# Optimization experiments

Hardware: AMD Instinct MI355X
Metric: run time of the kernel (lower is better)

The kernel has to match this reference:

```python
import jax, jax.numpy as jnp
import numpy as np

ALPHA = 0.2          # LeakyReLU negative slope (Alpha)
NEG_INF = -9e15      # mask value used by pygat-style GAT


def _masked_attention(Wh, a_src, a_dst, mask):
    """Wh: [H,N,d], a_src/a_dst: [H,d], mask: [N,N] (nonzero = edge).
    Returns attention-aggregated features [H,N,d]."""
    f_src = jnp.einsum('hnd,hd->hn', Wh, a_src)   # [H,N]
    f_dst = jnp.einsum('hnd,hd->hn', Wh, a_dst)   # [H,N]
    e = jax.nn.leaky_relu(f_src[:, :, None] + f_dst[:, None, :], ALPHA)  # [H,N,N]
    e = jnp.where(mask[None, :, :] > 0, e, NEG_INF)
    att = jax.nn.softmax(e, axis=-1)              # masked softmax over neighbors
    return jnp.einsum('hnm,hmd->hnd', att, Wh)    # [H,N,d]


def setup_inputs() -> dict:
    key = jax.random.key(0)
    ks = jax.random.split(key, 8)
    N, F_in, D, H = 4096, 512, 64, 8
    x = jax.random.normal(ks[0], (N, F_in), dtype=jnp.float32)
    adj = jax.random.randint(ks[1], (N, N), 0, 2, dtype=jnp.int32)
    s = 0.1
    W = jax.random.normal(ks[2], (H, F_in, D), dtype=jnp.float32) * s
    a_src = jax.random.normal(ks[3], (H, D), dtype=jnp.float32) * s
    a_dst = jax.random.normal(ks[4], (H, D), dtype=jnp.float32) * s
    W_o = jax.random.normal(ks[5], (H * D, D), dtype=jnp.float32) * s
    ao_src = jax.random.normal(ks[6], (D,), dtype=jnp.float32) * s
    ao_dst = jax.random.normal(ks[7], (D,), dtype=jnp.float32) * s
    return {"x": x, "adj": adj, "W": W, "a_src": a_src, "a_dst": a_dst,
            "W_o": W_o, "ao_src": ao_src, "ao_dst": ao_dst}


def reference(x, adj, W, a_src, a_dst, W_o, ao_src, ao_dst):
    N = x.shape[0]
    # --- multi-head layer (concat=True: ELU per head, concat on feature dim) ---
    Wh = jnp.einsum('nf,hfd->hnd', x, W)                     # [H,N,d]
    h1 = jax.nn.elu(_masked_attention(Wh, a_src, a_dst, adj))  # [H,N,d]
    h_cat = jnp.transpose(h1, (1, 0, 2)).reshape(N, -1)      # [N, H*d]
    # --- output head (concat=False: no ELU inside layer) ---
    Who = (h_cat @ W_o)[None]                                # [1,N,d]
    h2 = _masked_attention(Who, ao_src[None], ao_dst[None], adj)[0]  # [N,d]
    # GAT.forward: activation (ELU) then log_softmax over dim=1
    return jax.nn.log_softmax(jax.nn.elu(h2), axis=1)
```

## Files before the change

### kernel.cpp

```cpp
#include <hip/hip_runtime.h>
#include <hip/hip_bf16.h>
#include <math.h>

#define N_NODES 4096
#define FDIM 512
#define D 64
#define H 8
#define NWORDS (N_NODES / 64)
#define S1 4
#define S2 16

typedef __attribute__((ext_vector_type(8))) short bf16x8;
typedef __attribute__((ext_vector_type(4))) float f32x4;
typedef __attribute__((ext_vector_type(8))) _Float16 f16x8;
typedef __attribute__((ext_vector_type(2))) _Float16 f16x2;
typedef __attribute__((ext_vector_type(4))) unsigned int u32x4;

__device__ inline short f2h(float x) {
    _Float16 h = (_Float16)x;
    return __builtin_bit_cast(short, h);
}
__device__ inline float h2f(unsigned short u) {
    return (float)__builtin_bit_cast(_Float16, u);
}
__device__ inline f16x2 bcH(unsigned int u) { return __builtin_bit_cast(f16x2, u); }

__device__ inline int sext_bit(unsigned int v, int j) {
#if defined(__has_builtin) && __has_builtin(__builtin_amdgcn_sbfe)
    return __builtin_amdgcn_sbfe((int)v, j, 1);
#else
    return ((int)(v << (31 - j))) >> 31;
#endif
}

__device__ inline unsigned fenc(float f) {
    unsigned u = __builtin_bit_cast(unsigned, f);
    return (u & 0x80000000u) ? ~u : (u | 0x80000000u);
}
__device__ inline float fdec(unsigned e) {
    unsigned u = (e & 0x80000000u) ? (e & 0x7FFFFFFFu) : ~e;
    return __builtin_bit_cast(float, u);
}

__device__ inline void gl2lds16(const void* g, void* l) {
#if defined(__has_builtin) && __has_builtin(__builtin_amdgcn_global_load_lds)
    __builtin_amdgcn_global_load_lds(
        (const __attribute__((address_space(1))) unsigned int*)g,
        (__attribute__((address_space(3))) unsigned int*)l, 16, 0, 0);
#else
    *(uint4*)l = *(const uint4*)g;
#endif
}

#define NB_BITS (N_NODES * N_NODES / 2048)
#define NB_X    (N_NODES * FDIM / 1024)
#define NB_W    (H * FDIM * D / 256)
#define NB_WO   (FDIM * D / 256)
__global__ void k_pre(const int* __restrict__ adj, const float* __restrict__ x,
                      const float* __restrict__ W, const float* __restrict__ Wo,
                      unsigned int* __restrict__ bits32, short* __restrict__ Xbf,
                      short* __restrict__ WF, short* __restrict__ WoF,
                      float* __restrict__ cm1, float* __restrict__ cm2,
                      unsigned* __restrict__ gmaxe1, unsigned* __restrict__ gmaxe2) {
    const int b = blockIdx.x, t = threadIdx.x;
    if (b == 0) {
        for (int i = t; i < H * D; i += 256) cm1[i] = 0.f;
        if (t < D) cm2[t] = 0.f;
        if (t < H) gmaxe1[t] = 0u;
        if (t == 0) gmaxe2[0] = 0u;
        return;
    }
    if (b < 1 + NB_BITS) {
        const int tid  = (b - 1) * 256 + t;
        const size_t e0 = (size_t)tid * 8;
        int4 a0 = *(const int4*)&adj[e0];
        int4 a1 = *(const int4*)&adj[e0 + 4];
        unsigned by = (unsigned)(a0.x != 0)       | ((unsigned)(a0.y != 0) << 1)
                    | ((unsigned)(a0.z != 0) << 2) | ((unsigned)(a0.w != 0) << 3)
                    | ((unsigned)(a1.x != 0) << 4) | ((unsigned)(a1.y != 0) << 5)
                    | ((unsigned)(a1.z != 0) << 6) | ((unsigned)(a1.w != 0) << 7);
        unsigned v = by | (__shfl_xor((int)by, 1) << 8);
        v = v | ((unsigned)__shfl_xor((int)v, 2) << 16);
        if ((t & 3) == 0) bits32[tid >> 2] = v;
        return;
    }
    if (b < 1 + NB_BITS + NB_X) {
        const size_t i4 = ((size_t)(b - 1 - NB_BITS) * 256 + t) * 4;
        float4 v = *(const float4*)&x[i4];
        ushort4 o;
        o.x = (unsigned short)f2h(v.x); o.y = (unsigned short)f2h(v.y);
        o.z = (unsigned short)f2h(v.z); o.w = (unsigned short)f2h(v.w);
        *(ushort4*)&Xbf[i4] = o;
        return;
    }
    if (b < 1 + NB_BITS + NB_X + NB_W) {
        const size_t idx = (size_t)(b - 1 - NB_BITS - NB_X) * 256 + t;
        const int d = idx & 63;
        const int k = (int)(idx >> 6) & 511;
        const int h = (int)(idx >> 15);
        WF[(((size_t)h * 64 + (k >> 3)) * 64 + d) * 8 + (k & 7)] = f2h(W[idx]);
        return;
    }
    {
        const size_t idx = (size_t)(b - 1 - NB_BITS - NB_X - NB_W) * 256 + t;
        const int d = idx & 63;
        const int k = (int)(idx >> 6);
        WoF[(((size_t)(k >> 3)) * 64 + d) * 8 + (k & 7)] = f2h(Wo[idx]);
    }
}

__global__ void __launch_bounds__(256) k_gemm(
    const short* __restrict__ Xbf, const short* __restrict__ WF,
    const float* __restrict__ av, const float* __restrict__ bv,
    short* __restrict__ WBout, float* __restrict__ fs, float* __restrict__ fd,
    unsigned* __restrict__ gmaxe, float* __restrict__ cm) {
    const int h  = blockIdx.y;
    const int i0 = blockIdx.x * 64;
    const int t = threadIdx.x, w = t >> 6, lane = t & 63;
    const int li = lane & 15, quad = lane >> 4, k0 = quad * 8;
    const int row_a = i0 + w * 16 + li;
    const short* __restrict__ Xr  = Xbf + (size_t)row_a * FDIM;
    const short* __restrict__ WFh = WF + (size_t)h * 64 * D * 8;

    f32x4 c0 = {0.f, 0.f, 0.f, 0.f}, c1 = c0, c2 = c0, c3 = c0;
    #pragma unroll 4
    for (int kt = 0; kt < FDIM; kt += 32) {
        f16x8 a = __builtin_bit_cast(f16x8, *(const bf16x8*)&Xr[kt + k0]);
        const short* bb = WFh + (size_t)((kt >> 3) + quad) * (D * 8) + li * 8;
        f16x8 b0 = __builtin_bit_cast(f16x8, *(const bf16x8*)(bb));
        f16x8 b1 = __builtin_bit_cast(f16x8, *(const bf16x8*)(bb + 128));
        f16x8 b2 = __builtin_bit_cast(f16x8, *(const bf16x8*)(bb + 256));
        f16x8 b3 = __builtin_bit_cast(f16x8, *(const bf16x8*)(bb + 384));
        c0 = __builtin_amdgcn_mfma_f32_16x16x32_f16(a, b0, c0, 0, 0, 0);
        c1 = __builtin_amdgcn_mfma_f32_16x16x32_f16(a, b1, c1, 0, 0, 0);
        c2 = __builtin_amdgcn_mfma_f32_16x16x32_f16(a, b2, c2, 0, 0, 0);
        c3 = __builtin_amdgcn_mfma_f32_16x16x32_f16(a, b3, c3, 0, 0, 0);
    }
    float av4[4], bv4[4];
    #pragma unroll
    for (int t4 = 0; t4 < 4; ++t4) {
        av4[t4] = av[h * D + t4 * 16 + li];
        bv4[t4] = bv[h * D + t4 * 16 + li];
    }
    float tiles[4][4];
    #pragma unroll
    for (int r = 0; r < 4; ++r) { tiles[0][r] = c0[r]; tiles[1][r] = c1[r]; tiles[2][r] = c2[r]; tiles[3][r] = c3[r]; }

    __shared__ float csum[4][64];
    __shared__ float red[4];
    float fdmax = -INFINITY;
    float s4[4] = {0.f, 0.f, 0.f, 0.f};

    #pragma unroll
    for (int r = 0; r < 4; ++r) {
        const int row = i0 + w * 16 + quad * 4 + r;
        float pa = 0.f, pb = 0.f;
        #pragma unroll
        for (int t4 = 0; t4 < 4; ++t4) {
            const float v = tiles[t4][r];
            const int d = t4 * 16 + li;
            WBout[((size_t)h * (N_NODES / 8) + (row >> 3)) * (D * 8) + d * 8 + (row & 7)] = f2h(v);
            pa += v * av4[t4];
            pb += v * bv4[t4];
            s4[t4] += v;
        }
        #pragma unroll
        for (int off = 1; off < 16; off <<= 1) {
            pa += __shfl_xor(pa, off);
            pb += __shfl_xor(pb, off);
        }
        if (li == 0) {
            fs[(size_t)h * N_NODES + row] = pa;
            fd[(size_t)h * N_NODES + row] = pb;
        }
        fdmax = fmaxf(fdmax, pb);
    }
    fdmax = fmaxf(fdmax, __shfl_xor(fdmax, 16));
    fdmax = fmaxf(fdmax, __shfl_xor(fdmax, 32));
    if (lane == 0) red[w] = fdmax;
    #pragma unroll
    for (int t4 = 0; t4 < 4; ++t4) {
        s4[t4] += __shfl_xor(s4[t4], 16);
        s4[t4] += __shfl_xor(s4[t4], 32);
    }
    if (quad == 0)
        #pragma unroll
        for (int t4 = 0; t4 < 4; ++t4) csum[w][t4 * 16 + li] = s4[t4];
    __syncthreads();
    if (t == 0)
        atomicMax(gmaxe + h, fenc(fmaxf(fmaxf(red[0], red[1]), fmaxf(red[2], red[3]))));
    if (t < 64)
        atomicAdd(&cm[h * D + t],
                  (csum[0][t] + csum[1][t] + csum[2][t] + csum[3][t]) * (1.f / (float)N_NODES));
}

__global__ void __launch_bounds__(128, 2) k_accum(
    const unsigned int* __restrict__ bits32,
    const short* __restrict__ WB,
    const float* __restrict__ fsb, const float* __restrict__ fdb,
    const unsigned* __restrict__ gmaxe,
    short* __restrict__ num, float* __restrict__ den, int kslab) {

    __shared__ __align__(16) short Bt[2][16 * 64 * 8];
    __shared__ __align__(16) short Esh[1024];
    __shared__ __align__(16) short Gsh[1024];

    const int h = blockIdx.y, i0 = blockIdx.x * 128, slab = blockIdx.z;
    const int t = threadIdx.x, w = t >> 6, lane = t & 63;
    const int li = lane & 15, quad = lane >> 4, k0 = quad * 8;
    const size_t ho = (size_t)h * N_NODES;
    const float  gm = fdec(gmaxe[h]);
    const float* __restrict__ fd = fdb + ho;
    const short* __restrict__ Bh = WB + (size_t)h * (N_NODES / 8) * D * 8;

    const int k_beg = slab * kslab;
    const int ntile = kslab / 128;

    auto stage = [&](int buf, int jtile) {
        const short* src = Bh + (size_t)(jtile >> 3) * (D * 8);
        #pragma unroll
        for (int p = 0; p < 8; ++p)
            gl2lds16(src + (size_t)(p * 128 + t) * 8, &Bt[buf][(p * 128 + t) * 8]);
    };

    int bito[4];
    #pragma unroll
    for (int f = 0; f < 4; ++f)
        bito[f] = (i0 + w * 64 + f * 16 + li) * (NWORDS * 2);
    uint4 bw[4];
    #pragma unroll
    for (int f = 0; f < 4; ++f)
        bw[f] = *(const uint4*)&bits32[(size_t)bito[f] + (k_beg >> 5)];
    stage(0, k_beg);
    for (int jj = t * 2; jj < kslab; jj += 256) {
        float2 f2 = *(const float2*)&fd[k_beg + jj];
        f16x2 ep = {(_Float16)__expf(f2.x - gm), (_Float16)__expf(f2.y - gm)};
        f16x2 gp = {(_Float16)__expf(0.2f * (f2.x - gm)),
                    (_Float16)__expf(0.2f * (f2.y - gm))};
        *(f16x2*)&Esh[jj] = ep;
        *(f16x2*)&Gsh[jj] = gp;
    }
    f16x2 Rp[4];
    #pragma unroll
    for (int f = 0; f < 4; ++f) {
        const float rv = __expf(-0.8f * (fsb[ho + i0 + w * 64 + f * 16 + li] + gm));
        const _Float16 rh = (_Float16)rv;
        Rp[f] = (f16x2){rh, rh};
    }

    f32x4 acc[4][4], c5[4];
    #pragma unroll
    for (int f = 0; f < 4; ++f) {
        #pragma unroll
        for (int q = 0; q < 4; ++q) acc[f][q] = (f32x4){0.f, 0.f, 0.f, 0.f};
        c5[f] = (f32x4){0.f, 0.f, 0.f, 0.f};
    }
    bf16x8 ones_;
    #pragma unroll
    for (int j = 0; j < 8; ++j) ones_[j] = (short)0x3C00;
    const f16x8 ones = __builtin_bit_cast(f16x8, ones_);

    __syncthreads();

    for (int tile = 0; tile < ntile; ++tile) {
        const int jt = k_beg + tile * 128;
        __builtin_amdgcn_s_barrier();
        if (tile > 0) {
            #pragma unroll
            for (int f = 0; f < 4; ++f)
                bw[f] = *(const uint4*)&bits32[(size_t)bito[f] + (jt >> 5)];
        }
        if (tile + 1 < ntile) {
            stage((tile + 1) & 1, jt + 128);
            asm volatile("s_waitcnt vmcnt(8)" ::: "memory");
        } else {
            asm volatile("s_waitcnt vmcnt(0)" ::: "memory");
        }
        __builtin_amdgcn_s_barrier();

        const short* Bl = Bt[tile & 1];
        const short* Ee = Esh + tile * 128;
        const short* Gg = Gsh + tile * 128;
        #pragma unroll
        for (int s = 0; s < 4; ++s) {
            const uint4 Eu = *(const uint4*)&Ee[s * 32 + k0];
            const uint4 Gu = *(const uint4*)&Gg[s * 32 + k0];
            f16x2 Ep[4] = {bcH(Eu.x), bcH(Eu.y), bcH(Eu.z), bcH(Eu.w)};
            f16x2 Gp[4] = {bcH(Gu.x), bcH(Gu.y), bcH(Gu.z), bcH(Gu.w)};
            const short* bb = Bl + (size_t)((s * 4 + quad) * 64 + li) * 8;
            f16x8 b0 = __builtin_bit_cast(f16x8, *(const bf16x8*)(bb));
            f16x8 b1 = __builtin_bit_cast(f16x8, *(const bf16x8*)(bb + 128));
            f16x8 b2 = __builtin_bit_cast(f16x8, *(const bf16x8*)(bb + 256));
            f16x8 b3 = __builtin_bit_cast(f16x8, *(const bf16x8*)(bb + 384));
            #pragma unroll
            for (int f = 0; f < 4; ++f) {
                const unsigned int wsel = (s == 0) ? bw[f].x : (s == 1) ? bw[f].y
                                        : (s == 2) ? bw[f].z : bw[f].w;
                const unsigned int byt = (wsel >> k0) & 0xFFu;
                u32x4 au;
                #pragma unroll
                for (int d2 = 0; d2 < 4; ++d2) {
                    const unsigned mw = (unsigned)__builtin_amdgcn_perm(
                        (unsigned)sext_bit(byt, 2 * d2 + 1),
                        (unsigned)sext_bit(byt, 2 * d2), 0x05040100u);
                    const f16x2 tv = Gp[d2] * Rp[f];
                    const f16x2 pv = __builtin_elementwise_max(Ep[d2], tv);
                    au[d2] = __builtin_bit_cast(unsigned, pv) & mw;
                }
                const f16x8 a = __builtin_bit_cast(f16x8, au);
                __builtin_amdgcn_s_setprio(1);
                acc[f][0] = __builtin_amdgcn_mfma_f32_16x16x32_f16(a, b0, acc[f][0], 0, 0, 0);
                acc[f][1] = __builtin_amdgcn_mfma_f32_16x16x32_f16(a, b1, acc[f][1], 0, 0, 0);
                acc[f][2] = __builtin_amdgcn_mfma_f32_16x16x32_f16(a, b2, acc[f][2], 0, 0, 0);
                acc[f][3] = __builtin_amdgcn_mfma_f32_16x16x32_f16(a, b3, acc[f][3], 0, 0, 0);
                c5[f]     = __builtin_amdgcn_mfma_f32_16x16x32_f16(a, ones, c5[f], 0, 0, 0);
                __builtin_amdgcn_s_setprio(0);
            }
        }
    }

    const size_t so = (size_t)(slab * gridDim.y + h);
    #pragma unroll
    for (int f = 0; f < 4; ++f) {
        #pragma unroll
        for (int t4 = 0; t4 < 4; ++t4)
            #pragma unroll
            for (int r = 0; r < 4; ++r) {
                const int row = i0 + w * 64 + f * 16 + quad * 4 + r;
                num[(so * N_NODES + row) * D + t4 * 16 + li] = f2h(acc[f][t4][r]);
            }
        if (li == 0)
            #pragma unroll
            for (int r = 0; r < 4; ++r)
                den[so * N_NODES + i0 + w * 64 + f * 16 + quad * 4 + r] = c5[f][r];
    }
}

__global__ void k_post1(const short* __restrict__ num, const float* __restrict__ den,
                        const float* __restrict__ colmean, short* __restrict__ hcat) {
    const int h   = blockIdx.y;
    const int i0  = blockIdx.x * 64;
    const int t   = threadIdx.x;
    const int row = i0 + (t >> 2);
    const int cb  = (t & 3) * 16;
    const size_t HN = (size_t)gridDim.y * N_NODES;
    const size_t r0 = (size_t)h * N_NODES + row;
    float dsum = 0.f;
    #pragma unroll
    for (int s = 0; s < S1; ++s) dsum += den[s * HN + r0];
    const bool  uni  = !(dsum > 0.f);
    const float linv = uni ? 0.f : 1.f / dsum;
    #pragma unroll
    for (int c = 0; c < 4; ++c) {
        const int col = cb + c * 4;
        float4 v = {0.f, 0.f, 0.f, 0.f};
        #pragma unroll
        for (int s = 0; s < S1; ++s) {
            ushort4 a = *(const ushort4*)&num[(s * HN + r0) * D + col];
            v.x += h2f(a.x); v.y += h2f(a.y); v.z += h2f(a.z); v.w += h2f(a.w);
        }
        v.x *= linv; v.y *= linv; v.z *= linv; v.w *= linv;
        if (uni) v = *(const float4*)&colmean[h * D + col];
        v.x = v.x > 0.f ? v.x : __expf(v.x) - 1.f;
        v.y = v.y > 0.f ? v.y : __expf(v.y) - 1.f;
        v.z = v.z > 0.f ? v.z : __expf(v.z) - 1.f;
        v.w = v.w > 0.f ? v.w : __expf(v.w) - 1.f;
        ushort4 o;
        o.x = (unsigned short)f2h(v.x); o.y = (unsigned short)f2h(v.y);
        o.z = (unsigned short)f2h(v.z); o.w = (unsigned short)f2h(v.w);
        *(ushort4*)&hcat[(size_t)row * (H * D) + h * D + col] = o;
    }
}

__global__ void k_lsm(const short* __restrict__ num, const float* __restrict__ den,
                      const float* __restrict__ cm, float* __restrict__ out) {
    const int n    = blockIdx.x * 4 + (threadIdx.x >> 6);
    const int lane = threadIdx.x & 63;
    float v = 0.f, ds = 0.f;
    #pragma unroll
    for (int s = 0; s < S2; ++s)
        v += h2f((unsigned short)num[((size_t)s * N_NODES + n) * D + lane]);
    #pragma unroll
    for (int s = 0; s < S2; ++s) ds += den[(size_t)s * N_NODES + n];
    v = (ds > 0.f) ? v / ds : cm[lane];
    v = v > 0.f ? v : __expf(v) - 1.f;
    float mx = v;
    #pragma unroll
    for (int off = 32; off > 0; off >>= 1) mx = fmaxf(mx, __shfl_xor(mx, off));
    float ex = __expf(v - mx);
    float sum = ex;
    #pragma unroll
    for (int off = 32; off > 0; off >>= 1) sum += __shfl_xor(sum, off);
    out[(size_t)n * D + lane] = (v - mx) - __logf(sum);
}

extern "C" void kernel_launch(void* const* d_in, const int* in_sizes, int n_in,
                              void* d_out, int out_size, void* d_ws, size_t ws_size,
                              hipStream_t stream) {
    const float* x      = (const float*)d_in[0];
    const int*   adj    = (const int*)d_in[1];
    const float* W      = (const float*)d_in[2];
    const float* a_src  = (const float*)d_in[3];
    const float* a_dst  = (const float*)d_in[4];
    const float* W_o    = (const float*)d_in[5];
    const float* ao_src = (const float*)d_in[6];
    const float* ao_dst = (const float*)d_in[7];
    float* out = (float*)d_out;

    char* wsp = (char*)d_ws;
    size_t off = 0;
    auto alloc = [&](size_t bytes) -> void* {
        void* p = wsp + off;
        off += (bytes + 255) & ~(size_t)255;
        return p;
    };
    unsigned* adj_bits = (unsigned*)alloc((size_t)N_NODES * NWORDS * 8);
    short*    Xbf   = (short*)alloc((size_t)N_NODES * FDIM * 2);
    short*    WF1   = (short*)alloc((size_t)H * 64 * D * 8 * 2);
    short*    WoF   = (short*)alloc((size_t)64 * D * 8 * 2);
    short*    WhB   = (short*)alloc((size_t)H * N_NODES * D * 2);
    float*    fs1   = (float*)alloc((size_t)H * N_NODES * 4);
    float*    fd1   = (float*)alloc((size_t)H * N_NODES * 4);
    unsigned* gme1  = (unsigned*)alloc((size_t)H * 4);
    float*    cm1   = (float*)alloc((size_t)H * D * 4);
    short*    num1  = (short*)alloc((size_t)S1 * H * N_NODES * D * 2);
    float*    den1  = (float*)alloc((size_t)S1 * H * N_NODES * 4);
    short*    hcat  = (short*)alloc((size_t)N_NODES * H * D * 2);
    short*    WhoB  = (short*)alloc((size_t)N_NODES * D * 2);
    float*    fs2   = (float*)alloc((size_t)N_NODES * 4);
    float*    fd2   = (float*)alloc((size_t)N_NODES * 4);
    unsigned* gme2  = (unsigned*)alloc(4);
    float*    cm2   = (float*)alloc((size_t)D * 4);
    short*    num2  = (short*)alloc((size_t)S2 * N_NODES * D * 2);
    float*    den2  = (float*)alloc((size_t)S2 * N_NODES * 4);

    k_pre  <<<dim3(1 + NB_BITS + NB_X + NB_W + NB_WO), dim3(256), 0, stream>>>(
        adj, x, W, W_o, adj_bits, Xbf, WF1, WoF, cm1, cm2, gme1, gme2);

    k_gemm <<<dim3(N_NODES / 64, H), dim3(256), 0, stream>>>(Xbf, WF1, a_src, a_dst,
                                                             WhB, fs1, fd1, gme1, cm1);
    k_accum<<<dim3(N_NODES / 128, H, S1), dim3(128), 0, stream>>>(adj_bits, WhB, fs1, fd1, gme1,
                                                                  num1, den1, N_NODES / S1);
    k_post1<<<dim3(N_NODES / 64, H), dim3(256), 0, stream>>>(num1, den1, cm1, hcat);

    k_gemm <<<dim3(N_NODES / 64, 1), dim3(256), 0, stream>>>(hcat, WoF, ao_src, ao_dst,
                                                             WhoB, fs2, fd2, gme2, cm2);
    k_accum<<<dim3(N_NODES / 128, 1, S2), dim3(128), 0, stream>>>(adj_bits, WhoB, fs2, fd2, gme2,
                                                                  num2, den2, N_NODES / S2);
    k_lsm  <<<dim3(N_NODES / 4), dim3(256), 0, stream>>>(num2, den2, cm2, out);
}
```

Baseline: 195.5 us.

## Drop split-K slabs and fuse normalization/ELU/log-softmax epilogues into accum kernels

Each attention-accumulation kernel now runs over all 4096 neighbours per row block instead of splitting K into slabs. The normalisation, ELU and (for the output layer) log-softmax are applied directly from registers. This removes the fp16 partial num/den buffers, their global write and readback, and the separate k_post1 and k_lsm launches. The cost is a much smaller grid (256 and 128 blocks of 2 waves each), which lowers occupancy and latency hiding. The per-tile pipelining is also simplified: the adjacency-bit loads now sit inside the loop and a full __syncthreads ends each tile.

```diff
diff --git a/kernel.cpp b/kernel.cpp
--- a/kernel.cpp
+++ b/kernel.cpp
@@ -7,8 +7,6 @@
 #define D 64
 #define H 8
 #define NWORDS (N_NODES / 64)
-#define S1 4
-#define S2 16
 
 typedef __attribute__((ext_vector_type(8))) short bf16x8;
 typedef __attribute__((ext_vector_type(4))) float f32x4;
@@ -194,27 +192,25 @@
                   (csum[0][t] + csum[1][t] + csum[2][t] + csum[3][t]) * (1.f / (float)N_NODES));
 }
 
-__global__ void __launch_bounds__(128, 2) k_accum(
+__global__ void __launch_bounds__(128, 2) k_accum1(
     const unsigned int* __restrict__ bits32,
     const short* __restrict__ WB,
     const float* __restrict__ fsb, const float* __restrict__ fdb,
-    const unsigned* __restrict__ gmaxe,
-    short* __restrict__ num, float* __restrict__ den, int kslab) {
+    const unsigned* __restrict__ gmaxe, const float* __restrict__ cm,
+    short* __restrict__ hcat) {
 
     __shared__ __align__(16) short Bt[2][16 * 64 * 8];
-    __shared__ __align__(16) short Esh[1024];
-    __shared__ __align__(16) short Gsh[1024];
-
-    const int h = blockIdx.y, i0 = blockIdx.x * 128, slab = blockIdx.z;
+    __shared__ __align__(16) short Esh[N_NODES];
+    __shared__ __align__(16) short Gsh[N_NODES];
+
+    const int h = blockIdx.y, i0 = blockIdx.x * 128;
     const int t = threadIdx.x, w = t >> 6, lane = t & 63;
     const int li = lane & 15, quad = lane >> 4, k0 = quad * 8;
     const size_t ho = (size_t)h * N_NODES;
     const float  gm = fdec(gmaxe[h]);
     const float* __restrict__ fd = fdb + ho;
     const short* __restrict__ Bh = WB + (size_t)h * (N_NODES / 8) * D * 8;
-
-    const int k_beg = slab * kslab;
-    const int ntile = kslab / 128;
+    const int ntile = N_NODES / 128;
 
     auto stage = [&](int buf, int jtile) {
         const short* src = Bh + (size_t)(jtile >> 3) * (D * 8);
@@ -227,13 +223,9 @@
     #pragma unroll
     for (int f = 0; f < 4; ++f)
         bito[f] = (i0 + w * 64 + f * 16 + li) * (NWORDS * 2);
-    uint4 bw[4];
-    #pragma unroll
-    for (int f = 0; f < 4; ++f)
-        bw[f] = *(const uint4*)&bits32[(size_t)bito[f] + (k_beg >> 5)];
-    stage(0, k_beg);
-    for (int jj = t * 2; jj < kslab; jj += 256) {
-        float2 f2 = *(const float2*)&fd[k_beg + jj];
+    stage(0, 0);
+    for (int jj = t * 2; jj < N_NODES; jj += 256) {
+        float2 f2 = *(const float2*)&fd[jj];
         f16x2 ep = {(_Float16)__expf(f2.x - gm), (_Float16)__expf(f2.y - gm)};
         f16x2 gp = {(_Float16)__expf(0.2f * (f2.x - gm)),
                     (_Float16)__expf(0.2f * (f2.y - gm))};
@@ -263,24 +255,17 @@
     __syncthreads();
 
     for (int tile = 0; tile < ntile; ++tile) {
-        const int jt = k_beg + tile * 128;
-        __builtin_amdgcn_s_barrier();
-        if (tile > 0) {
-            #pragma unroll
-            for (int f = 0; f < 4; ++f)
-                bw[f] = *(const uint4*)&bits32[(size_t)bito[f] + (jt >> 5)];
-        }
-        if (tile + 1 < ntile) {
-            stage((tile + 1) & 1, jt + 128);
-            asm volatile("s_waitcnt vmcnt(8)" ::: "memory");
-        } else {
-            asm volatile("s_waitcnt vmcnt(0)" ::: "memory");
-        }
-        __builtin_amdgcn_s_barrier();
+        const int jt = tile * 128;
+        if (tile + 1 < ntile) stage((tile + 1) & 1, jt + 128);
+
+        uint4 bw[4];
+        #pragma unroll
+        for (int f = 0; f < 4; ++f)
+            bw[f] = *(const uint4*)&bits32[(size_t)bito[f] + (jt >> 5)];
 
         const short* Bl = Bt[tile & 1];
-        const short* Ee = Esh + tile * 128;
-        const short* Gg = Gsh + tile * 128;
+        const short* Ee = Esh + jt;
+        const short* Gg = Gsh + jt;
         #pragma unroll
         for (int s = 0; s < 4; ++s) {
             const uint4 Eu = *(const uint4*)&Ee[s * 32 + k0];
@@ -317,81 +302,159 @@
                 __builtin_amdgcn_s_setprio(0);
             }
         }
-    }
-
-    const size_t so = (size_t)(slab * gridDim.y + h);
+        __syncthreads();
+    }
+
+    float cmv[4];
+    #pragma unroll
+    for (int t4 = 0; t4 < 4; ++t4) cmv[t4] = cm[h * D + t4 * 16 + li];
     #pragma unroll
     for (int f = 0; f < 4; ++f) {
         #pragma unroll
+        for (int r = 0; r < 4; ++r) {
+            const int row = i0 + w * 64 + f * 16 + quad * 4 + r;
+            const float den = c5[f][r];
+            const bool  uni = !(den > 0.f);
+            const float linv = uni ? 0.f : 1.f / den;
+            #pragma unroll
+            for (int t4 = 0; t4 < 4; ++t4) {
+                float v = acc[f][t4][r] * linv;
+                if (uni) v = cmv[t4];
+                v = v > 0.f ? v : __expf(v) - 1.f;
+                hcat[(size_t)row * (H * D) + h * D + t4 * 16 + li] = f2h(v);
+            }
+        }
+    }
+}
+
+__global__ void __launch_bounds__(128, 2) k_accum2(
+    const unsigned int* __restrict__ bits32,
+    const short* __restrict__ WB,
+    const float* __restrict__ fsb, const float* __restrict__ fdb,
+    const unsigned* __restrict__ gmaxe, const float* __restrict__ cm,
+    float* __restrict__ out) {
+
+    __shared__ __align__(16) short Bt[2][16 * 64 * 8];
+    __shared__ __align__(16) short Esh[N_NODES];
+    __shared__ __align__(16) short Gsh[N_NODES];
+
+    const int i0 = blockIdx.x * 32;
+    const int t = threadIdx.x, w = t >> 6, lane = t & 63;
+    const int li = lane & 15, quad = lane >> 4, k0 = quad * 8;
+    const float gm = fdec(gmaxe[0]);
+    const int ntile = N_NODES / 128;
+
+    auto stage = [&](int buf, int jtile) {
+        const short* src = WB + (size_t)(jtile >> 3) * (D * 8);
+        #pragma unroll
+        for (int p = 0; p < 8; ++p)
+            gl2lds16(src + (size_t)(p * 128 + t) * 8, &Bt[buf][(p * 128 + t) * 8]);
+    };
+
+    const int bito = (i0 + w * 16 + li) * (NWORDS * 2);
+    stage(0, 0);
+    for (int jj = t * 2; jj < N_NODES; jj += 256) {
+        float2 f2 = *(const float2*)&fdb[jj];
+        f16x2 ep = {(_Float16)__expf(f2.x - gm), (_Float16)__expf(f2.y - gm)};
+        f16x2 gp = {(_Float16)__expf(0.2f * (f2.x - gm)),
+                    (_Float16)__expf(0.2f * (f2.y - gm))};
+        *(f16x2*)&Esh[jj] = ep;
+        *(f16x2*)&Gsh[jj] = gp;
+    }
+    f16x2 Rp;
+    {
+        const float rv = __expf(-0.8f * (fsb[i0 + w * 16 + li] + gm));
+        const _Float16 rh = (_Float16)rv;
+        Rp = (f16x2){rh, rh};
+    }
+
+    f32x4 acc[4], c5;
+    #pragma unroll
+    for (int q = 0; q < 4; ++q) acc[q] = (f32x4){0.f, 0.f, 0.f, 0.f};
+    c5 = (f32x4){0.f, 0.f, 0.f, 0.f};
+    bf16x8 ones_;
+    #pragma unroll
+    for (int j = 0; j < 8; ++j) ones_[j] = (short)0x3C00;
+    const f16x8 ones = __builtin_bit_cast(f16x8, ones_);
+
+    __syncthreads();
+
+    for (int tile = 0; tile < ntile; ++tile) {
+        const int jt = tile * 128;
+        if (tile + 1 < ntile) stage((tile + 1) & 1, jt + 128);
+
+        uint4 bw = *(const uint4*)&bits32[(size_t)bito + (jt >> 5)];
+
+        const short* Bl = Bt[tile & 1];
+        const short* Ee = Esh + jt;
+        const short* Gg = Gsh + jt;
+        #pragma unroll
+        for (int s = 0; s < 4; ++s) {
+            const uint4 Eu = *(const uint4*)&Ee[s * 32 + k0];
+            const uint4 Gu = *(const uint4*)&Gg[s * 32 + k0];
+            f16x2 Ep[4] = {bcH(Eu.x), bcH(Eu.y), bcH(Eu.z), bcH(Eu.w)};
+            f16x2 Gp[4] = {bcH(Gu.x), bcH(Gu.y), bcH(Gu.z), bcH(Gu.w)};
+            const short* bb = Bl + (size_t)((s * 4 + quad) * 64 + li) * 8;
+            f16x8 b0 = __builtin_bit_cast(f16x8, *(const bf16x8*)(bb));
+            f16x8 b1 = __builtin_bit_cast(f16x8, *(const bf16x8*)(bb + 128));
+            f16x8 b2 = __builtin_bit_cast(f16x8, *(const bf16x8*)(bb + 256));
+            f16x8 b3 = __builtin_bit_cast(f16x8, *(const bf16x8*)(bb + 384));
+            const unsigned int wsel = (s == 0) ? bw.x : (s == 1) ? bw.y
+                                    : (s == 2) ? bw.z : bw.w;
+            const unsigned int byt = (wsel >> k0) & 0xFFu;
+            u32x4 au;
+            #pragma unroll
+            for (int d2 = 0; d2 < 4; ++d2) {
+                const unsigned mw = (unsigned)__builtin_amdgcn_perm(
+                    (unsigned)sext_bit(byt, 2 * d2 + 1),
+                    (unsigned)sext_bit(byt, 2 * d2), 0x05040100u);
+                const f16x2 tv = Gp[d2] * Rp;
+                const f16x2 pv = __builtin_elementwise_max(Ep[d2], tv);
+                au[d2] = __builtin_bit_cast(unsigned, pv) & mw;
+            }
+            const f16x8 a = __builtin_bit_cast(f16x8, au);
+            __builtin_amdgcn_s_setprio(1);
+            acc[0] = __builtin_amdgcn_mfma_f32_16x16x32_f16(a, b0, acc[0], 0, 0, 0);
+            acc[1] = __builtin_amdgcn_mfma_f32_16x16x32_f16(a, b1, acc[1], 0, 0, 0);
+            acc[2] = __builtin_amdgcn_mfma_f32_16x16x32_f16(a, b2, acc[2], 0, 0, 0);
+            acc[3] = __builtin_amdgcn_mfma_f32_16x16x32_f16(a, b3, acc[3], 0, 0, 0);
+            c5     = __builtin_amdgcn_mfma_f32_16x16x32_f16(a, ones, c5, 0, 0, 0);
+            __builtin_amdgcn_s_setprio(0);
+        }
+        __syncthreads();
+    }
+
+    float cmv[4];
+    #pragma unroll
+    for (int t4 = 0; t4 < 4; ++t4) cmv[t4] = cm[t4 * 16 + li];
+    #pragma unroll
+    for (int r = 0; r < 4; ++r) {
+        const int row = i0 + w * 16 + quad * 4 + r;
+        const float den = c5[r];
+        const bool  uni = !(den > 0.f);
+        const float linv = uni ? 0.f : 1.f / den;
+        float v[4];
+        float mx = -INFINITY;
+        #pragma unroll
+        for (int t4 = 0; t4 < 4; ++t4) {
+            float x = acc[t4][r] * linv;
+            if (uni) x = cmv[t4];
+            x = x > 0.f ? x : __expf(x) - 1.f;
+            v[t4] = x;
+            mx = fmaxf(mx, x);
+        }
+        #pragma unroll
+        for (int off = 1; off < 16; off <<= 1) mx = fmaxf(mx, __shfl_xor(mx, off));
+        float sum = 0.f;
+        #pragma unroll
+        for (int t4 = 0; t4 < 4; ++t4) sum += __expf(v[t4] - mx);
+        #pragma unroll
+        for (int off = 1; off < 16; off <<= 1) sum += __shfl_xor(sum, off);
+        const float ls = __logf(sum);
+        #pragma unroll
         for (int t4 = 0; t4 < 4; ++t4)
-            #pragma unroll
-            for (int r = 0; r < 4; ++r) {
-                const int row = i0 + w * 64 + f * 16 + quad * 4 + r;
-                num[(so * N_NODES + row) * D + t4 * 16 + li] = f2h(acc[f][t4][r]);
-            }
-        if (li == 0)
-            #pragma unroll
-            for (int r = 0; r < 4; ++r)
-                den[so * N_NODES + i0 + w * 64 + f * 16 + quad * 4 + r] = c5[f][r];
-    }
-}
-
-__global__ void k_post1(const short* __restrict__ num, const float* __restrict__ den,
-                        const float* __restrict__ colmean, short* __restrict__ hcat) {
-    const int h   = blockIdx.y;
-    const int i0  = blockIdx.x * 64;
-    const int t   = threadIdx.x;
-    const int row = i0 + (t >> 2);
-    const int cb  = (t & 3) * 16;
-    const size_t HN = (size_t)gridDim.y * N_NODES;
-    const size_t r0 = (size_t)h * N_NODES + row;
-    float dsum = 0.f;
-    #pragma unroll
-    for (int s = 0; s < S1; ++s) dsum += den[s * HN + r0];
-    const bool  uni  = !(dsum > 0.f);
-    const float linv = uni ? 0.f : 1.f / dsum;
-    #pragma unroll
-    for (int c = 0; c < 4; ++c) {
-        const int col = cb + c * 4;
-        float4 v = {0.f, 0.f, 0.f, 0.f};
-        #pragma unroll
-        for (int s = 0; s < S1; ++s) {
-            ushort4 a = *(const ushort4*)&num[(s * HN + r0) * D + col];
-            v.x += h2f(a.x); v.y += h2f(a.y); v.z += h2f(a.z); v.w += h2f(a.w);
-        }
-        v.x *= linv; v.y *= linv; v.z *= linv; v.w *= linv;
-        if (uni) v = *(const float4*)&colmean[h * D + col];
-        v.x = v.x > 0.f ? v.x : __expf(v.x) - 1.f;
-        v.y = v.y > 0.f ? v.y : __expf(v.y) - 1.f;
-        v.z = v.z > 0.f ? v.z : __expf(v.z) - 1.f;
-        v.w = v.w > 0.f ? v.w : __expf(v.w) - 1.f;
-        ushort4 o;
-        o.x = (unsigned short)f2h(v.x); o.y = (unsigned short)f2h(v.y);
-        o.z = (unsigned short)f2h(v.z); o.w = (unsigned short)f2h(v.w);
-        *(ushort4*)&hcat[(size_t)row * (H * D) + h * D + col] = o;
-    }
-}
-
-__global__ void k_lsm(const short* __restrict__ num, const float* __restrict__ den,
-                      const float* __restrict__ cm, float* __restrict__ out) {
-    const int n    = blockIdx.x * 4 + (threadIdx.x >> 6);
-    const int lane = threadIdx.x & 63;
-    float v = 0.f, ds = 0.f;
-    #pragma unroll
-    for (int s = 0; s < S2; ++s)
-        v += h2f((unsigned short)num[((size_t)s * N_NODES + n) * D + lane]);
-    #pragma unroll
-    for (int s = 0; s < S2; ++s) ds += den[(size_t)s * N_NODES + n];
-    v = (ds > 0.f) ? v / ds : cm[lane];
-    v = v > 0.f ? v : __expf(v) - 1.f;
-    float mx = v;
-    #pragma unroll
-    for (int off = 32; off > 0; off >>= 1) mx = fmaxf(mx, __shfl_xor(mx, off));
-    float ex = __expf(v - mx);
-    float sum = ex;
-    #pragma unroll
-    for (int off = 32; off > 0; off >>= 1) sum += __shfl_xor(sum, off);
-    out[(size_t)n * D + lane] = (v - mx) - __logf(sum);
+            out[(size_t)row * D + t4 * 16 + li] = (v[t4] - mx) - ls;
+    }
 }
 
 extern "C" void kernel_launch(void* const* d_in, const int* in_sizes, int n_in,
@@ -423,29 +486,23 @@
     float*    fd1   = (float*)alloc((size_t)H * N_NODES * 4);
     unsigned* gme1  = (unsigned*)alloc((size_t)H * 4);
     float*    cm1   = (float*)alloc((size_t)H * D * 4);
-    short*    num1  = (short*)alloc((size_t)S1 * H * N_NODES * D * 2);
-    float*    den1  = (float*)alloc((size_t)S1 * H * N_NODES * 4);
     short*    hcat  = (short*)alloc((size_t)N_NODES * H * D * 2);
     short*    WhoB  = (short*)alloc((size_t)N_NODES * D * 2);
     float*    fs2   = (float*)alloc((size_t)N_NODES * 4);
     float*    fd2   = (float*)alloc((size_t)N_NODES * 4);
     unsigned* gme2  = (unsigned*)alloc(4);
     float*    cm2   = (float*)alloc((size_t)D * 4);
-    short*    num2  = (short*)alloc((size_t)S2 * N_NODES * D * 2);
-    float*    den2  = (float*)alloc((size_t)S2 * N_NODES * 4);
 
     k_pre  <<<dim3(1 + NB_BITS + NB_X + NB_W + NB_WO), dim3(256), 0, stream>>>(
         adj, x, W, W_o, adj_bits, Xbf, WF1, WoF, cm1, cm2, gme1, gme2);
 
-    k_gemm <<<dim3(N_NODES / 64, H), dim3(256), 0, stream>>>(Xbf, WF1, a_src, a_dst,
-                                                             WhB, fs1, fd1, gme1, cm1);
-    k_accum<<<dim3(N_NODES / 128, H, S1), dim3(128), 0, stream>>>(adj_bits, WhB, fs1, fd1, gme1,
-                                                                  num1, den1, N_NODES / S1);
-    k_post1<<<dim3(N_NODES / 64, H), dim3(256), 0, stream>>>(num1, den1, cm1, hcat);
-
-    k_gemm <<<dim3(N_NODES / 64, 1), dim3(256), 0, stream>>>(hcat, WoF, ao_src, ao_dst,
-                                                             WhoB, fs2, fd2, gme2, cm2);
-    k_accum<<<dim3(N_NODES / 128, 1, S2), dim3(128), 0, stream>>>(adj_bits, WhoB, fs2, fd2, gme2,
-                                                                  num2, den2, N_NODES / S2);
-    k_lsm  <<<dim3(N_NODES / 4), dim3(256), 0, stream>>>(num2, den2, cm2, out);
-}
+    k_gemm  <<<dim3(N_NODES / 64, H), dim3(256), 0, stream>>>(Xbf, WF1, a_src, a_dst,
+                                                              WhB, fs1, fd1, gme1, cm1);
+    k_accum1<<<dim3(N_NODES / 128, H), dim3(128), 0, stream>>>(adj_bits, WhB, fs1, fd1,
+                                                               gme1, cm1, hcat);
+
+    k_gemm  <<<dim3(N_NODES / 64, 1), dim3(256), 0, stream>>>(hcat, WoF, ao_src, ao_dst,
+                                                              WhoB, fs2, fd2, gme2, cm2);
+    k_accum2<<<dim3(N_NODES / 32), dim3(128), 0, stream>>>(adj_bits, WhoB, fs2, fd2,
+                                                           gme2, cm2, out);
+}
```

Measured after the change: 260.7 us. 33.3% more time.

## Fuse post-processing and output GEMM into accumulation kernels via last-block counters

Applied to the files above, without the earlier changes.

Replaces the separate post1, second GEMM and log-softmax launches with last-arriving-block epilogues in the accumulation kernels, using atomic counters and threadfences. The main loop is also reworked: the async-copy waitcnt and double-barrier scheme becomes a single syncthreads per tile, with the bitmask loaded inside the loop. The second-layer split grows from 16 to 32 slabs. This cuts launch overhead and kernel-boundary idle time, at the cost of serialized tail work in a few blocks and a possibly weaker load/compute overlap in the inner loop.

```diff
diff --git a/kernel.cpp b/kernel.cpp
--- a/kernel.cpp
+++ b/kernel.cpp
@@ -8,7 +8,8 @@
 #define H 8
 #define NWORDS (N_NODES / 64)
 #define S1 4
-#define S2 16
+#define S2 32
+#define NTHR 128
 
 typedef __attribute__((ext_vector_type(8))) short bf16x8;
 typedef __attribute__((ext_vector_type(4))) float f32x4;
@@ -51,6 +52,12 @@
     *(uint4*)l = *(const uint4*)g;
 #endif
 }
+
+union Smem {
+    struct { short Bt[2][8192]; short Esh[1024]; short Gsh[1024]; } a;
+    struct { float csum[128]; float red[2]; } g;
+    struct { float dsum[128]; } p;
+};
 
 #define NB_BITS (N_NODES * N_NODES / 2048)
 #define NB_X    (N_NODES * FDIM / 1024)
@@ -61,13 +68,15 @@
                       unsigned int* __restrict__ bits32, short* __restrict__ Xbf,
                       short* __restrict__ WF, short* __restrict__ WoF,
                       float* __restrict__ cm1, float* __restrict__ cm2,
-                      unsigned* __restrict__ gmaxe1, unsigned* __restrict__ gmaxe2) {
+                      unsigned* __restrict__ gmaxe1, unsigned* __restrict__ gmaxe2,
+                      int* __restrict__ cnt) {
     const int b = blockIdx.x, t = threadIdx.x;
     if (b == 0) {
         for (int i = t; i < H * D; i += 256) cm1[i] = 0.f;
         if (t < D) cm2[t] = 0.f;
         if (t < H) gmaxe1[t] = 0u;
         if (t == 0) gmaxe2[0] = 0u;
+        for (int i = t; i < 320; i += 256) cnt[i] = 0;
         return;
     }
     if (b < 1 + NB_BITS) {
@@ -194,56 +203,41 @@
                   (csum[0][t] + csum[1][t] + csum[2][t] + csum[3][t]) * (1.f / (float)N_NODES));
 }
 
-__global__ void __launch_bounds__(128, 2) k_accum(
-    const unsigned int* __restrict__ bits32,
-    const short* __restrict__ WB,
-    const float* __restrict__ fsb, const float* __restrict__ fdb,
-    const unsigned* __restrict__ gmaxe,
-    short* __restrict__ num, float* __restrict__ den, int kslab) {
-
-    __shared__ __align__(16) short Bt[2][16 * 64 * 8];
-    __shared__ __align__(16) short Esh[1024];
-    __shared__ __align__(16) short Gsh[1024];
-
-    const int h = blockIdx.y, i0 = blockIdx.x * 128, slab = blockIdx.z;
-    const int t = threadIdx.x, w = t >> 6, lane = t & 63;
+__device__ __forceinline__ void accum_slab(
+    const unsigned int* __restrict__ bits32, const short* __restrict__ Bh,
+    const float* __restrict__ fsh, const float* __restrict__ fdh,
+    float gm, int i0, int k_beg, int kslab,
+    short* __restrict__ num, float* __restrict__ den, size_t so,
+    int t, Smem& sm)
+{
+    const int w = t >> 6, lane = t & 63;
     const int li = lane & 15, quad = lane >> 4, k0 = quad * 8;
-    const size_t ho = (size_t)h * N_NODES;
-    const float  gm = fdec(gmaxe[h]);
-    const float* __restrict__ fd = fdb + ho;
-    const short* __restrict__ Bh = WB + (size_t)h * (N_NODES / 8) * D * 8;
-
-    const int k_beg = slab * kslab;
     const int ntile = kslab / 128;
 
     auto stage = [&](int buf, int jtile) {
         const short* src = Bh + (size_t)(jtile >> 3) * (D * 8);
         #pragma unroll
         for (int p = 0; p < 8; ++p)
-            gl2lds16(src + (size_t)(p * 128 + t) * 8, &Bt[buf][(p * 128 + t) * 8]);
+            gl2lds16(src + (size_t)(p * 128 + t) * 8, &sm.a.Bt[buf][(p * 128 + t) * 8]);
     };
 
     int bito[4];
     #pragma unroll
     for (int f = 0; f < 4; ++f)
         bito[f] = (i0 + w * 64 + f * 16 + li) * (NWORDS * 2);
-    uint4 bw[4];
-    #pragma unroll
-    for (int f = 0; f < 4; ++f)
-        bw[f] = *(const uint4*)&bits32[(size_t)bito[f] + (k_beg >> 5)];
     stage(0, k_beg);
-    for (int jj = t * 2; jj < kslab; jj += 256) {
-        float2 f2 = *(const float2*)&fd[k_beg + jj];
+    for (int jj = t * 2; jj < kslab; jj += 2 * NTHR) {
+        float2 f2 = *(const float2*)&fdh[k_beg + jj];
         f16x2 ep = {(_Float16)__expf(f2.x - gm), (_Float16)__expf(f2.y - gm)};
         f16x2 gp = {(_Float16)__expf(0.2f * (f2.x - gm)),
                     (_Float16)__expf(0.2f * (f2.y - gm))};
-        *(f16x2*)&Esh[jj] = ep;
-        *(f16x2*)&Gsh[jj] = gp;
+        *(f16x2*)&sm.a.Esh[jj] = ep;
+        *(f16x2*)&sm.a.Gsh[jj] = gp;
     }
     f16x2 Rp[4];
     #pragma unroll
     for (int f = 0; f < 4; ++f) {
-        const float rv = __expf(-0.8f * (fsb[ho + i0 + w * 64 + f * 16 + li] + gm));
+        const float rv = __expf(-0.8f * (fsh[i0 + w * 64 + f * 16 + li] + gm));
         const _Float16 rh = (_Float16)rv;
         Rp[f] = (f16x2){rh, rh};
     }
@@ -264,23 +258,16 @@
 
     for (int tile = 0; tile < ntile; ++tile) {
         const int jt = k_beg + tile * 128;
-        __builtin_amdgcn_s_barrier();
-        if (tile > 0) {
-            #pragma unroll
-            for (int f = 0; f < 4; ++f)
-                bw[f] = *(const uint4*)&bits32[(size_t)bito[f] + (jt >> 5)];
-        }
-        if (tile + 1 < ntile) {
-            stage((tile + 1) & 1, jt + 128);
-            asm volatile("s_waitcnt vmcnt(8)" ::: "memory");
-        } else {
-            asm volatile("s_waitcnt vmcnt(0)" ::: "memory");
-        }
-        __builtin_amdgcn_s_barrier();
-
-        const short* Bl = Bt[tile & 1];
-        const short* Ee = Esh + tile * 128;
-        const short* Gg = Gsh + tile * 128;
+        if (tile + 1 < ntile) stage((tile + 1) & 1, jt + 128);
+
+        uint4 bw[4];
+        #pragma unroll
+        for (int f = 0; f < 4; ++f)
+            bw[f] = *(const uint4*)&bits32[(size_t)bito[f] + (jt >> 5)];
+
+        const short* Bl = sm.a.Bt[tile & 1];
+        const short* Ee = sm.a.Esh + tile * 128;
+        const short* Gg = sm.a.Gsh + tile * 128;
         #pragma unroll
         for (int s = 0; s < 4; ++s) {
             const uint4 Eu = *(const uint4*)&Ee[s * 32 + k0];
@@ -317,9 +304,9 @@
                 __builtin_amdgcn_s_setprio(0);
             }
         }
-    }
-
-    const size_t so = (size_t)(slab * gridDim.y + h);
+        __syncthreads();
+    }
+
     #pragma unroll
     for (int f = 0; f < 4; ++f) {
         #pragma unroll
@@ -336,62 +323,197 @@
     }
 }
 
-__global__ void k_post1(const short* __restrict__ num, const float* __restrict__ den,
-                        const float* __restrict__ colmean, short* __restrict__ hcat) {
-    const int h   = blockIdx.y;
-    const int i0  = blockIdx.x * 64;
-    const int t   = threadIdx.x;
-    const int row = i0 + (t >> 2);
-    const int cb  = (t & 3) * 16;
-    const size_t HN = (size_t)gridDim.y * N_NODES;
-    const size_t r0 = (size_t)h * N_NODES + row;
-    float dsum = 0.f;
-    #pragma unroll
-    for (int s = 0; s < S1; ++s) dsum += den[s * HN + r0];
-    const bool  uni  = !(dsum > 0.f);
-    const float linv = uni ? 0.f : 1.f / dsum;
-    #pragma unroll
-    for (int c = 0; c < 4; ++c) {
-        const int col = cb + c * 4;
-        float4 v = {0.f, 0.f, 0.f, 0.f};
-        #pragma unroll
-        for (int s = 0; s < S1; ++s) {
-            ushort4 a = *(const ushort4*)&num[(s * HN + r0) * D + col];
-            v.x += h2f(a.x); v.y += h2f(a.y); v.z += h2f(a.z); v.w += h2f(a.w);
-        }
-        v.x *= linv; v.y *= linv; v.z *= linv; v.w *= linv;
-        if (uni) v = *(const float4*)&colmean[h * D + col];
-        v.x = v.x > 0.f ? v.x : __expf(v.x) - 1.f;
-        v.y = v.y > 0.f ? v.y : __expf(v.y) - 1.f;
-        v.z = v.z > 0.f ? v.z : __expf(v.z) - 1.f;
-        v.w = v.w > 0.f ? v.w : __expf(v.w) - 1.f;
-        ushort4 o;
-        o.x = (unsigned short)f2h(v.x); o.y = (unsigned short)f2h(v.y);
-        o.z = (unsigned short)f2h(v.z); o.w = (unsigned short)f2h(v.w);
-        *(ushort4*)&hcat[(size_t)row * (H * D) + h * D + col] = o;
-    }
-}
-
-__global__ void k_lsm(const short* __restrict__ num, const float* __restrict__ den,
-                      const float* __restrict__ cm, float* __restrict__ out) {
-    const int n    = blockIdx.x * 4 + (threadIdx.x >> 6);
-    const int lane = threadIdx.x & 63;
-    float v = 0.f, ds = 0.f;
-    #pragma unroll
-    for (int s = 0; s < S2; ++s)
-        v += h2f((unsigned short)num[((size_t)s * N_NODES + n) * D + lane]);
-    #pragma unroll
-    for (int s = 0; s < S2; ++s) ds += den[(size_t)s * N_NODES + n];
-    v = (ds > 0.f) ? v / ds : cm[lane];
-    v = v > 0.f ? v : __expf(v) - 1.f;
-    float mx = v;
-    #pragma unroll
-    for (int off = 32; off > 0; off >>= 1) mx = fmaxf(mx, __shfl_xor(mx, off));
-    float ex = __expf(v - mx);
-    float sum = ex;
-    #pragma unroll
-    for (int off = 32; off > 0; off >>= 1) sum += __shfl_xor(sum, off);
-    out[(size_t)n * D + lane] = (v - mx) - __logf(sum);
+__device__ __forceinline__ void gemm_block128(
+    const short* __restrict__ Xsrc, const short* __restrict__ WFh,
+    const float* __restrict__ av, const float* __restrict__ bv,
+    short* __restrict__ WBh, float* __restrict__ fsh, float* __restrict__ fdh,
+    unsigned* __restrict__ gmaxp, float* __restrict__ cmh,
+    int i0, int t, Smem& sm)
+{
+    const int w = t >> 6, lane = t & 63;
+    const int li = lane & 15, quad = lane >> 4, k0 = quad * 8;
+    const int row_a = i0 + w * 16 + li;
+    const short* __restrict__ Xr = Xsrc + (size_t)row_a * FDIM;
+
+    f32x4 c0 = {0.f, 0.f, 0.f, 0.f}, c1 = c0, c2 = c0, c3 = c0;
+    #pragma unroll 4
+    for (int kt = 0; kt < FDIM; kt += 32) {
+        f16x8 a = __builtin_bit_cast(f16x8, *(const bf16x8*)&Xr[kt + k0]);
+        const short* bb = WFh + (size_t)((kt >> 3) + quad) * (D * 8) + li * 8;
+        f16x8 b0 = __builtin_bit_cast(f16x8, *(const bf16x8*)(bb));
+        f16x8 b1 = __builtin_bit_cast(f16x8, *(const bf16x8*)(bb + 128));
+        f16x8 b2 = __builtin_bit_cast(f16x8, *(const bf16x8*)(bb + 256));
+        f16x8 b3 = __builtin_bit_cast(f16x8, *(const bf16x8*)(bb + 384));
+        c0 = __builtin_amdgcn_mfma_f32_16x16x32_f16(a, b0, c0, 0, 0, 0);
+        c1 = __builtin_amdgcn_mfma_f32_16x16x32_f16(a, b1, c1, 0, 0, 0);
+        c2 = __builtin_amdgcn_mfma_f32_16x16x32_f16(a, b2, c2, 0, 0, 0);
+        c3 = __builtin_amdgcn_mfma_f32_16x16x32_f16(a, b3, c3, 0, 0, 0);
+    }
+    float av4[4], bv4[4];
+    #pragma unroll
+    for (int t4 = 0; t4 < 4; ++t4) {
+        av4[t4] = av[t4 * 16 + li];
+        bv4[t4] = bv[t4 * 16 + li];
+    }
+    float tiles[4][4];
+    #pragma unroll
+    for (int r = 0; r < 4; ++r) { tiles[0][r] = c0[r]; tiles[1][r] = c1[r]; tiles[2][r] = c2[r]; tiles[3][r] = c3[r]; }
+
+    float fdmax = -INFINITY;
+    float s4[4] = {0.f, 0.f, 0.f, 0.f};
+    #pragma unroll
+    for (int r = 0; r < 4; ++r) {
+        const int row = i0 + w * 16 + quad * 4 + r;
+        float pa = 0.f, pb = 0.f;
+        #pragma unroll
+        for (int t4 = 0; t4 < 4; ++t4) {
+            const float v = tiles[t4][r];
+            const int d = t4 * 16 + li;
+            WBh[((size_t)(row >> 3)) * (D * 8) + d * 8 + (row & 7)] = f2h(v);
+            pa += v * av4[t4];
+            pb += v * bv4[t4];
+            s4[t4] += v;
+        }
+        #pragma unroll
+        for (int off = 1; off < 16; off <<= 1) {
+            pa += __shfl_xor(pa, off);
+            pb += __shfl_xor(pb, off);
+        }
+        if (li == 0) {
+            fsh[row] = pa;
+            fdh[row] = pb;
+        }
+        fdmax = fmaxf(fdmax, pb);
+    }
+    fdmax = fmaxf(fdmax, __shfl_xor(fdmax, 16));
+    fdmax = fmaxf(fdmax, __shfl_xor(fdmax, 32));
+    if (lane == 0) sm.g.red[w] = fdmax;
+    #pragma unroll
+    for (int t4 = 0; t4 < 4; ++t4) {
+        s4[t4] += __shfl_xor(s4[t4], 16);
+        s4[t4] += __shfl_xor(s4[t4], 32);
+    }
+    if (quad == 0)
+        #pragma unroll
+        for (int t4 = 0; t4 < 4; ++t4) sm.g.csum[w * 64 + t4 * 16 + li] = s4[t4];
+    __syncthreads();
+    if (t == 0)
+        atomicMax(gmaxp, fenc(fmaxf(sm.g.red[0], sm.g.red[1])));
+    if (t < 64)
+        atomicAdd(&cmh[t], (sm.g.csum[t] + sm.g.csum[64 + t]) * (1.f / (float)N_NODES));
+    __syncthreads();
+}
+
+__global__ void __launch_bounds__(NTHR, 2) k_accum1m(
+    const unsigned int* __restrict__ bits32, const short* __restrict__ WhB,
+    const float* __restrict__ fs1, const float* __restrict__ fd1,
+    const unsigned* __restrict__ gme1, const float* __restrict__ cm1,
+    short* __restrict__ num1, float* __restrict__ den1, short* __restrict__ hcat,
+    const short* __restrict__ WoF, const float* __restrict__ ao_src,
+    const float* __restrict__ ao_dst, short* __restrict__ WhoB,
+    float* __restrict__ fs2, float* __restrict__ fd2,
+    unsigned* __restrict__ gme2, float* __restrict__ cm2,
+    int* __restrict__ cnt)
+{
+    __shared__ Smem sm;
+    __shared__ int tk1, tk2;
+    const int b = blockIdx.x, t = threadIdx.x;
+    const int rb = b & 31, h = (b >> 5) & 7, slab = b >> 8;
+
+    accum_slab(bits32, WhB + (size_t)h * (N_NODES / 8) * (D * 8),
+               fs1 + (size_t)h * N_NODES, fd1 + (size_t)h * N_NODES,
+               fdec(gme1[h]), rb * 128, slab * (N_NODES / S1), N_NODES / S1,
+               num1, den1, (size_t)slab * H + h, t, sm);
+
+    __syncthreads();
+    __threadfence();
+    if (t == 0) tk1 = atomicAdd(&cnt[rb * 8 + h], 1);
+    __syncthreads();
+    if (tk1 != S1 - 1) return;
+    __threadfence();
+
+    {
+        const int row = rb * 128 + t;
+        float ds = 0.f;
+        #pragma unroll
+        for (int s = 0; s < S1; ++s)
+            ds += den1[((size_t)s * H + h) * N_NODES + row];
+        sm.p.dsum[t] = ds;
+    }
+    __syncthreads();
+    #pragma unroll 1
+    for (int it = 0; it < 64; ++it) {
+        const int rr  = it * 2 + (t >> 6);
+        const int row = rb * 128 + rr;
+        const int col = t & 63;
+        float v = 0.f;
+        #pragma unroll
+        for (int s = 0; s < S1; ++s)
+            v += h2f((unsigned short)num1[(((size_t)s * H + h) * N_NODES + row) * D + col]);
+        const float ds = sm.p.dsum[rr];
+        v = (ds > 0.f) ? v / ds : cm1[h * D + col];
+        v = v > 0.f ? v : __expf(v) - 1.f;
+        hcat[(size_t)row * (H * D) + h * D + col] = f2h(v);
+    }
+
+    __syncthreads();
+    __threadfence();
+    if (t == 0) tk2 = atomicAdd(&cnt[256 + rb], 1);
+    __syncthreads();
+    if (tk2 != H - 1) return;
+    __threadfence();
+    #pragma unroll 1
+    for (int p = 0; p < 4; ++p)
+        gemm_block128(hcat, WoF, ao_src, ao_dst, WhoB, fs2, fd2, gme2, cm2,
+                      rb * 128 + p * 32, t, sm);
+}
+
+__global__ void __launch_bounds__(NTHR, 2) k_accum2m(
+    const unsigned int* __restrict__ bits32, const short* __restrict__ WhoB,
+    const float* __restrict__ fs2, const float* __restrict__ fd2,
+    const unsigned* __restrict__ gme2, const float* __restrict__ cm2,
+    short* __restrict__ num2, float* __restrict__ den2,
+    float* __restrict__ out, int* __restrict__ cnt)
+{
+    __shared__ Smem sm;
+    __shared__ int tk;
+    const int b = blockIdx.x, t = threadIdx.x;
+    const int rb = b & 31, slab = b >> 5;
+
+    accum_slab(bits32, WhoB, fs2, fd2, fdec(gme2[0]),
+               rb * 128, slab * (N_NODES / S2), N_NODES / S2,
+               num2, den2, (size_t)slab, t, sm);
+
+    __syncthreads();
+    __threadfence();
+    if (t == 0) tk = atomicAdd(&cnt[288 + rb], 1);
+    __syncthreads();
+    if (tk != S2 - 1) return;
+    __threadfence();
+
+    #pragma unroll 1
+    for (int it = 0; it < 64; ++it) {
+        const int rr  = it * 2 + (t >> 6);
+        const int row = rb * 128 + rr;
+        const int col = t & 63;
+        float v = 0.f, ds = 0.f;
+        #pragma unroll
+        for (int s = 0; s < S2; ++s)
+            v += h2f((unsigned short)num2[((size_t)s * N_NODES + row) * D + col]);
+        #pragma unroll
+        for (int s = 0; s < S2; ++s)
+            ds += den2[(size_t)s * N_NODES + row];
+        v = (ds > 0.f) ? v / ds : cm2[col];
+        v = v > 0.f ? v : __expf(v) - 1.f;
+        float mx = v;
+        #pragma unroll
+        for (int off = 32; off > 0; off >>= 1) mx = fmaxf(mx, __shfl_xor(mx, off));
+        float ex = __expf(v - mx);
+        float sum = ex;
+        #pragma unroll
+        for (int off = 32; off > 0; off >>= 1) sum += __shfl_xor(sum, off);
+        out[(size_t)row * D + col] = (v - mx) - __logf(sum);
+    }
 }
 
 extern "C" void kernel_launch(void* const* d_in, const int* in_sizes, int n_in,
@@ -433,19 +555,18 @@
     float*    cm2   = (float*)alloc((size_t)D * 4);
     short*    num2  = (short*)alloc((size_t)S2 * N_NODES * D * 2);
     float*    den2  = (float*)alloc((size_t)S2 * N_NODES * 4);
-
-    k_pre  <<<dim3(1 + NB_BITS + NB_X + NB_W + NB_WO), dim3(256), 0, stream>>>(
-        adj, x, W, W_o, adj_bits, Xbf, WF1, WoF, cm1, cm2, gme1, gme2);
-
-    k_gemm <<<dim3(N_NODES / 64, H), dim3(256), 0, stream>>>(Xbf, WF1, a_src, a_dst,
-                                                             WhB, fs1, fd1, gme1, cm1);
-    k_accum<<<dim3(N_NODES / 128, H, S1), dim3(128), 0, stream>>>(adj_bits, WhB, fs1, fd1, gme1,
-                                                                  num1, den1, N_NODES / S1);
-    k_post1<<<dim3(N_NODES / 64, H), dim3(256), 0, stream>>>(num1, den1, cm1, hcat);
-
-    k_gemm <<<dim3(N_NODES / 64, 1), dim3(256), 0, stream>>>(hcat, WoF, ao_src, ao_dst,
-                                                             WhoB, fs2, fd2, gme2, cm2);
-    k_accum<<<dim3(N_NODES / 128, 1, S2), dim3(128), 0, stream>>>(adj_bits, WhoB, fs2, fd2, gme2,
-                                                                  num2, den2, N_NODES / S2);
-    k_lsm  <<<dim3(N_NODES / 4), dim3(256), 0, stream>>>(num2, den2, cm2, out);
-}
+    int*      cnt   = (int*)alloc((size_t)320 * 4);
+
+    k_pre   <<<dim3(1 + NB_BITS + NB_X + NB_W + NB_WO), dim3(256), 0, stream>>>(
+        adj, x, W, W_o, adj_bits, Xbf, WF1, WoF, cm1, cm2, gme1, gme2, cnt);
+
+    k_gemm  <<<dim3(N_NODES / 64, H), dim3(256), 0, stream>>>(Xbf, WF1, a_src, a_dst,
+                                                              WhB, fs1, fd1, gme1, cm1);
+
+    k_accum1m<<<dim3(32 * H * S1), dim3(NTHR), 0, stream>>>(
+        adj_bits, WhB, fs1, fd1, gme1, cm1, num1, den1, hcat,
+        WoF, ao_src, ao_dst, WhoB, fs2, fd2, gme2, cm2, cnt);
+
+    k_accum2m<<<dim3(32 * S2), dim3(NTHR), 0, stream>>>(
+        adj_bits, WhoB, fs2, fd2, gme2, cm2, num2, den2, out, cnt);
+}
```

Result: slower. 505.6 us (+158.6%).
